# Optimization experiments

Hardware: AMD Instinct MI355X
Metric: run time of the kernel (lower is better)

The kernel has to match this reference:

```python
import jax, jax.numpy as jnp
import numpy as np

IN_F, OUT_F = 128, 128
R, LEV, N = 2, 2, 8192
JD = (R - 1) * LEV + 1  # 3 filter levels


def setup_inputs() -> dict:
    key = jax.random.key(0)
    ks = jax.random.split(key, 7)
    x = jax.random.normal(ks[0], (N, IN_F), dtype=jnp.float32)
    d_list = jax.random.uniform(ks[1], (JD, N), dtype=jnp.float32)
    U = jax.random.normal(ks[2], (N, N), dtype=jnp.float32)
    Vt = jax.random.normal(ks[3], (N, N), dtype=jnp.float32)
    # learned params
    bound = float(np.sqrt(6.0 / (IN_F + OUT_F)))  # xavier_uniform
    weight = jax.random.uniform(ks[4], (IN_F, OUT_F), dtype=jnp.float32, minval=-bound, maxval=bound)
    filt = jax.random.uniform(ks[5], (JD, N), dtype=jnp.float32, minval=0.9, maxval=1.1)
    bias = jnp.zeros((OUT_F,), dtype=jnp.float32)
    return {"x": x, "d_list": d_list, "U": U, "Vt": Vt, "weight": weight, "filt": filt, "bias": bias}


def reference(x, d_list, U, Vt, weight, filt, bias):
    # Original loop: sum_j U @ ((d_j * f_j * d_j)[:, None] * (Vt @ (x @ W)))
    # By linearity this equals U @ ((sum_j d_j^2 * f_j)[:, None] * (Vt @ (x @ W)))
    # -- same math, with Vt@xw computed once and U applied once.
    xw = x @ weight                                  # [N, out]
    Vxw = Vt @ xw                                    # [N, out]
    scale = jnp.sum(d_list * filt * d_list, axis=0)  # [N]
    out = U @ (scale[:, None] * Vxw)                 # [N, out]
    return out + bias
```

## Files before the change

### kernel.cpp

```cpp
#include <hip/hip_runtime.h>

typedef short s8v __attribute__((ext_vector_type(8)));
typedef float f32x4 __attribute__((ext_vector_type(4)));
typedef unsigned short u16x4 __attribute__((ext_vector_type(4)));

#define KC 64
#define PAD 72

__device__ __forceinline__ unsigned short f2bf(float x) {
    unsigned int u = __float_as_uint(x);
    u += 0x7fffu + ((u >> 16) & 1u);
    return (unsigned short)(u >> 16);
}

__device__ __forceinline__ s8v cvt_frag(const float4 lo, const float4 hi) {
    s8v r;
    r[0] = (short)f2bf(lo.x); r[1] = (short)f2bf(lo.y);
    r[2] = (short)f2bf(lo.z); r[3] = (short)f2bf(lo.w);
    r[4] = (short)f2bf(hi.x); r[5] = (short)f2bf(hi.y);
    r[6] = (short)f2bf(hi.z); r[7] = (short)f2bf(hi.w);
    return r;
}

__device__ __forceinline__ void gemm_core(
    const float* __restrict__ A, int lda,
    const unsigned short* __restrict__ Bt, int ldb,
    int mbase, int k0, int klen, f32x4 acc[2][4])
{
    const int t    = threadIdx.x;
    const int w    = t >> 6;
    const int lane = t & 63;
    const int quad = lane >> 4;
    const int l16  = lane & 15;
    const int mh   = w >> 1;
    const int nh   = w & 1;

    const float* rA0 = A + (size_t)(mbase + mh * 32 + l16) * lda + k0 + quad * 8;
    const float* rA1 = rA0 + (size_t)16 * lda;
    const unsigned short* rB = Bt + (size_t)(nh * 64 + l16) * ldb + k0 + quad * 8;
    const size_t bstep = (size_t)16 * ldb;

    float4 a[2][2][2][2];
    s8v    b[2][2][4];
    const int nchunks = klen / KC;

#define LOADC(s, c) do { const size_t o = (size_t)(c) * KC;                    \
        _Pragma("unroll")                                                      \
        for (int kk = 0; kk < 2; ++kk) {                                       \
            a[s][0][kk][0] = *(const float4*)(rA0 + o + kk * 32);              \
            a[s][0][kk][1] = *(const float4*)(rA0 + o + kk * 32 + 4);          \
            a[s][1][kk][0] = *(const float4*)(rA1 + o + kk * 32);              \
            a[s][1][kk][1] = *(const float4*)(rA1 + o + kk * 32 + 4);          \
        }                                                                      \
        _Pragma("unroll")                                                      \
        for (int kk = 0; kk < 2; ++kk)                                         \
            _Pragma("unroll")                                                  \
            for (int ct = 0; ct < 4; ++ct)                                     \
                b[s][kk][ct] = *(const s8v*)(rB + ct * bstep + o + kk * 32);   \
    } while (0)

#define ITER(p)                                                                \
    {                                                                          \
        _Pragma("unroll")                                                      \
        for (int kk = 0; kk < 2; ++kk) {                                       \
            s8v af0 = cvt_frag(a[p][0][kk][0], a[p][0][kk][1]);                \
            s8v af1 = cvt_frag(a[p][1][kk][0], a[p][1][kk][1]);                \
            _Pragma("unroll")                                                  \
            for (int ct = 0; ct < 4; ++ct) {                                   \
                acc[0][ct] = __builtin_amdgcn_mfma_f32_16x16x32_bf16(          \
                    af0, b[p][kk][ct], acc[0][ct], 0, 0, 0);                   \
                acc[1][ct] = __builtin_amdgcn_mfma_f32_16x16x32_bf16(          \
                    af1, b[p][kk][ct], acc[1][ct], 0, 0, 0);                   \
            }                                                                  \
        }                                                                      \
        if (c + 2 < nchunks) LOADC(p, c + 2);                                  \
    }

    LOADC(0, 0);
    if (nchunks > 1) LOADC(1, 1);
    int c = 0;
    while (true) {
        ITER(0)
        if (++c == nchunks) break;
        ITER(1)
        if (++c == nchunks) break;
    }
#undef ITER
#undef LOADC
}

__global__ __launch_bounds__(256, 2) void gemm_kernel(
    const float* __restrict__ A, int lda,
    const unsigned short* __restrict__ Bt, int ldb,
    float* __restrict__ C, int klen)
{
    f32x4 acc[2][4];
    #pragma unroll
    for (int rt = 0; rt < 2; ++rt)
        #pragma unroll
        for (int ct = 0; ct < 4; ++ct)
            acc[rt][ct] = (f32x4){0.f, 0.f, 0.f, 0.f};

    const int mbase = blockIdx.x * 64;
    gemm_core(A, lda, Bt, ldb, mbase, blockIdx.y * klen, klen, acc);

    C += (size_t)blockIdx.y * 8192 * 128;
    const int t = threadIdx.x;
    const int lane = t & 63, w = t >> 6;
    const int quad = lane >> 4, l16 = lane & 15;
    const int mh = w >> 1, nh = w & 1;
    #pragma unroll
    for (int rt = 0; rt < 2; ++rt) {
        const int row0 = mbase + mh * 32 + rt * 16 + quad * 4;
        #pragma unroll
        for (int ct = 0; ct < 4; ++ct) {
            const int col = nh * 64 + ct * 16 + l16;
            #pragma unroll
            for (int i = 0; i < 4; ++i)
                C[(size_t)(row0 + i) * 128 + col] = acc[rt][ct][i];
        }
    }
}

__global__ __launch_bounds__(256, 2) void gemm_xw_kernel(
    const float* __restrict__ x, const unsigned short* __restrict__ Wt,
    unsigned short* __restrict__ out)
{
    f32x4 acc[2][4];
    #pragma unroll
    for (int rt = 0; rt < 2; ++rt)
        #pragma unroll
        for (int ct = 0; ct < 4; ++ct)
            acc[rt][ct] = (f32x4){0.f, 0.f, 0.f, 0.f};

    const int mbase = blockIdx.x * 64;
    gemm_core(x, 128, Wt, 128, mbase, 0, 128, acc);

    const int t = threadIdx.x;
    const int lane = t & 63, w = t >> 6;
    const int quad = lane >> 4, l16 = lane & 15;
    const int mh = w >> 1, nh = w & 1;
    #pragma unroll
    for (int rt = 0; rt < 2; ++rt) {
        const int r0 = mbase + mh * 32 + rt * 16 + quad * 4;
        #pragma unroll
        for (int ct = 0; ct < 4; ++ct) {
            const int f = nh * 64 + ct * 16 + l16;
            u16x4 v;
            v[0] = f2bf(acc[rt][ct][0]); v[1] = f2bf(acc[rt][ct][1]);
            v[2] = f2bf(acc[rt][ct][2]); v[3] = f2bf(acc[rt][ct][3]);
            *(u16x4*)&out[(size_t)f * 8192 + r0] = v;
        }
    }
}

__global__ __launch_bounds__(256) void tkern(
    const float* __restrict__ a, int nslabs,
    const float* __restrict__ dl, const float* __restrict__ ft,
    unsigned short* __restrict__ out, int nrows, int mode)
{
    __shared__ __align__(16) unsigned short L[128 * PAD];
    const int t    = threadIdx.x;
    const int kb   = blockIdx.x * 64;
    const int kloc = t >> 2;
    const int fseg = (t & 3) * 32;
    const int k    = kb + kloc;
    const size_t slab = (size_t)nrows * 128;

    float s = 1.0f;
    if (mode) {
        float s0 = 0.f;
        #pragma unroll
        for (int j = 0; j < 3; ++j) {
            float d = dl[(size_t)j * nrows + k];
            s0 += d * d * ft[(size_t)j * nrows + k];
        }
        s = s0;
    }
    const float* ap = a + (size_t)k * 128 + fseg;
    #pragma unroll
    for (int i = 0; i < 8; ++i) {
        float4 v = *(const float4*)(ap + i * 4);
        for (int sl = 1; sl < nslabs; ++sl) {
            float4 u = *(const float4*)(ap + sl * slab + i * 4);
            v.x += u.x; v.y += u.y; v.z += u.z; v.w += u.w;
        }
        const int fb = fseg + i * 4;
        L[(fb + 0) * PAD + kloc] = f2bf(v.x * s);
        L[(fb + 1) * PAD + kloc] = f2bf(v.y * s);
        L[(fb + 2) * PAD + kloc] = f2bf(v.z * s);
        L[(fb + 3) * PAD + kloc] = f2bf(v.w * s);
    }
    __syncthreads();
    const int f    = t >> 1;
    const int half = (t & 1) * 32;
    unsigned short* op = out + (size_t)f * nrows + kb + half;
    #pragma unroll
    for (int i = 0; i < 4; ++i) {
        *(s8v*)(op + i * 8) = *(const s8v*)&L[f * PAD + half + i * 8];
    }
}

__global__ __launch_bounds__(256) void addbias_kernel(
    const float* __restrict__ p, const float* __restrict__ bias,
    float* __restrict__ out)
{
    const size_t e = ((size_t)blockIdx.x * 256 + threadIdx.x) * 4;
    const size_t slab = (size_t)8192 * 128;
    float4 r = *(const float4*)(bias + (e & 127));
    #pragma unroll
    for (int s = 0; s < 4; ++s) {
        float4 x = *(const float4*)(p + s * slab + e);
        r.x += x.x; r.y += x.y; r.z += x.z; r.w += x.w;
    }
    *(float4*)(out + e) = r;
}

extern "C" void kernel_launch(void* const* d_in, const int* in_sizes, int n_in,
                              void* d_out, int out_size, void* d_ws, size_t ws_size,
                              hipStream_t stream)
{
    const float* x  = (const float*)d_in[0];
    const float* dl = (const float*)d_in[1];
    const float* U  = (const float*)d_in[2];
    const float* Vt = (const float*)d_in[3];
    const float* W  = (const float*)d_in[4];
    const float* ft = (const float*)d_in[5];
    const float* bs = (const float*)d_in[6];
    float* out = (float*)d_out;

    const int N = 8192;
    const int SPLITK = 4;
    char* ws = (char*)d_ws;
    unsigned short* Wt  = (unsigned short*)(ws);
    unsigned short* xwt = (unsigned short*)(ws + (64 << 10));
    unsigned short* yt  = (unsigned short*)(ws + (64 << 10) + (2 << 20));
    float* bufA = (float*)(ws + (64 << 10) + (4 << 20));
    float* bufB = (float*)(ws + (64 << 10) + (20 << 20));

    tkern<<<dim3(2), 256, 0, stream>>>(W, 1, nullptr, nullptr, Wt, 128, 0);
    gemm_xw_kernel<<<dim3(N / 64), 256, 0, stream>>>(x, Wt, xwt);
    gemm_kernel<<<dim3(N / 64, SPLITK), 256, 0, stream>>>(Vt, N, xwt, N, bufB, N / SPLITK);
    tkern<<<dim3(N / 64), 256, 0, stream>>>(bufB, SPLITK, dl, ft, yt, N, 1);
    gemm_kernel<<<dim3(N / 64, SPLITK), 256, 0, stream>>>(U, N, yt, N, bufA, N / SPLITK);
    addbias_kernel<<<dim3((N * 128) / (256 * 4)), 256, 0, stream>>>(bufA, bs, out);
}
```

Measured before the change: 671.8 us.

## Stage GEMM tiles through LDS ring with direct global-to-LDS loads

Replaces register-prefetched global loads with a three-stage LDS ring filled by global_load_lds DMA, using XOR-swizzled layouts to avoid bank conflicts, and halves the K chunk to fit. Each wave then reads A (fp32) and B (bf16) fragments from LDS, converts A to bf16 and issues MFMAs, synchronised by explicit waitcnt plus barrier. The aim is to lower register pressure and the cost of the loads on these memory-bound skinny GEMMs. The price is a block barrier on every chunk and 48KB of LDS per block, which may limit occupancy.

Result: faster. 612.4 us (-8.8%).

```diff
diff --git a/kernel.cpp b/kernel.cpp
--- a/kernel.cpp
+++ b/kernel.cpp
@@ -4,7 +4,7 @@
 typedef float f32x4 __attribute__((ext_vector_type(4)));
 typedef unsigned short u16x4 __attribute__((ext_vector_type(4)));
 
-#define KC 64
+#define KC 32
 #define PAD 72
 
 __device__ __forceinline__ unsigned short f2bf(float x) {
@@ -13,20 +13,29 @@
     return (unsigned short)(u >> 16);
 }
 
-__device__ __forceinline__ s8v cvt_frag(const float4 lo, const float4 hi) {
+__device__ __forceinline__ s8v cvt8(const f32x4 lo, const f32x4 hi) {
     s8v r;
-    r[0] = (short)f2bf(lo.x); r[1] = (short)f2bf(lo.y);
-    r[2] = (short)f2bf(lo.z); r[3] = (short)f2bf(lo.w);
-    r[4] = (short)f2bf(hi.x); r[5] = (short)f2bf(hi.y);
-    r[6] = (short)f2bf(hi.z); r[7] = (short)f2bf(hi.w);
+    r[0] = (short)f2bf(lo[0]); r[1] = (short)f2bf(lo[1]);
+    r[2] = (short)f2bf(lo[2]); r[3] = (short)f2bf(lo[3]);
+    r[4] = (short)f2bf(hi[0]); r[5] = (short)f2bf(hi[1]);
+    r[6] = (short)f2bf(hi[2]); r[7] = (short)f2bf(hi[3]);
     return r;
 }
 
-__device__ __forceinline__ void gemm_core(
+__device__ __forceinline__ void gl2lds16(const void* g, void* l) {
+    __builtin_amdgcn_global_load_lds(
+        (const __attribute__((address_space(1))) unsigned int*)g,
+        (__attribute__((address_space(3))) unsigned int*)l, 16, 0, 0);
+}
+
+template<int EPI>
+__global__ __launch_bounds__(256, 2) void gemm_dma(
     const float* __restrict__ A, int lda,
     const unsigned short* __restrict__ Bt, int ldb,
-    int mbase, int k0, int klen, f32x4 acc[2][4])
-{
+    void* __restrict__ Cout, int klen, int Mtot)
+{
+    __shared__ __align__(16) unsigned char ring[3][16384];
+
     const int t    = threadIdx.x;
     const int w    = t >> 6;
     const int lane = t & 63;
@@ -35,65 +44,40 @@
     const int mh   = w >> 1;
     const int nh   = w & 1;
 
-    const float* rA0 = A + (size_t)(mbase + mh * 32 + l16) * lda + k0 + quad * 8;
-    const float* rA1 = rA0 + (size_t)16 * lda;
-    const unsigned short* rB = Bt + (size_t)(nh * 64 + l16) * ldb + k0 + quad * 8;
-    const size_t bstep = (size_t)16 * ldb;
-
-    float4 a[2][2][2][2];
-    s8v    b[2][2][4];
+    const int mbase   = blockIdx.x * 64;
+    const int k0      = blockIdx.y * klen;
     const int nchunks = klen / KC;
 
-#define LOADC(s, c) do { const size_t o = (size_t)(c) * KC;                    \
-        _Pragma("unroll")                                                      \
-        for (int kk = 0; kk < 2; ++kk) {                                       \
-            a[s][0][kk][0] = *(const float4*)(rA0 + o + kk * 32);              \
-            a[s][0][kk][1] = *(const float4*)(rA0 + o + kk * 32 + 4);          \
-            a[s][1][kk][0] = *(const float4*)(rA1 + o + kk * 32);              \
-            a[s][1][kk][1] = *(const float4*)(rA1 + o + kk * 32 + 4);          \
-        }                                                                      \
-        _Pragma("unroll")                                                      \
-        for (int kk = 0; kk < 2; ++kk)                                         \
-            _Pragma("unroll")                                                  \
-            for (int ct = 0; ct < 4; ++ct)                                     \
-                b[s][kk][ct] = *(const s8v*)(rB + ct * bstep + o + kk * 32);   \
+    int arow[2], aoff[2];
+    #pragma unroll
+    for (int j = 0; j < 2; ++j) {
+        const int r = (j * 4 + w) * 8 + (lane >> 3);
+        arow[j] = r;
+        aoff[j] = (((lane & 7) ^ (r & 7)) * 4);
+    }
+    int bnrow[2], bnoff[2];
+    #pragma unroll
+    for (int j = 0; j < 2; ++j) {
+        const int n = (j * 4 + w) * 16 + (lane >> 2);
+        bnrow[j] = n;
+        bnoff[j] = (((lane & 3) ^ (n & 3)) * 8);
+    }
+    const float* Abase = A + (size_t)mbase * lda + k0;
+    const int ldsoff0 = (0 * 4 + w) * 1024 + lane * 16;
+    const int ldsoff1 = (1 * 4 + w) * 1024 + lane * 16;
+
+#define ISSUE(s, c) do {                                                       \
+        const int co_ = (c) * KC;                                              \
+        gl2lds16(Abase + (size_t)arow[0] * lda + co_ + aoff[0],                \
+                 &ring[s][ldsoff0]);                                           \
+        gl2lds16(Abase + (size_t)arow[1] * lda + co_ + aoff[1],                \
+                 &ring[s][ldsoff1]);                                           \
+        gl2lds16(Bt + (size_t)bnrow[0] * ldb + k0 + co_ + bnoff[0],            \
+                 &ring[s][8192 + ldsoff0]);                                    \
+        gl2lds16(Bt + (size_t)bnrow[1] * ldb + k0 + co_ + bnoff[1],            \
+                 &ring[s][8192 + ldsoff1]);                                    \
     } while (0)
 
-#define ITER(p)                                                                \
-    {                                                                          \
-        _Pragma("unroll")                                                      \
-        for (int kk = 0; kk < 2; ++kk) {                                       \
-            s8v af0 = cvt_frag(a[p][0][kk][0], a[p][0][kk][1]);                \
-            s8v af1 = cvt_frag(a[p][1][kk][0], a[p][1][kk][1]);                \
-            _Pragma("unroll")                                                  \
-            for (int ct = 0; ct < 4; ++ct) {                                   \
-                acc[0][ct] = __builtin_amdgcn_mfma_f32_16x16x32_bf16(          \
-                    af0, b[p][kk][ct], acc[0][ct], 0, 0, 0);                   \
-                acc[1][ct] = __builtin_amdgcn_mfma_f32_16x16x32_bf16(          \
-                    af1, b[p][kk][ct], acc[1][ct], 0, 0, 0);                   \
-            }                                                                  \
-        }                                                                      \
-        if (c + 2 < nchunks) LOADC(p, c + 2);                                  \
-    }
-
-    LOADC(0, 0);
-    if (nchunks > 1) LOADC(1, 1);
-    int c = 0;
-    while (true) {
-        ITER(0)
-        if (++c == nchunks) break;
-        ITER(1)
-        if (++c == nchunks) break;
-    }
-#undef ITER
-#undef LOADC
-}
-
-__global__ __launch_bounds__(256, 2) void gemm_kernel(
-    const float* __restrict__ A, int lda,
-    const unsigned short* __restrict__ Bt, int ldb,
-    float* __restrict__ C, int klen)
-{
     f32x4 acc[2][4];
     #pragma unroll
     for (int rt = 0; rt < 2; ++rt)
@@ -101,55 +85,72 @@
         for (int ct = 0; ct < 4; ++ct)
             acc[rt][ct] = (f32x4){0.f, 0.f, 0.f, 0.f};
 
-    const int mbase = blockIdx.x * 64;
-    gemm_core(A, lda, Bt, ldb, mbase, blockIdx.y * klen, klen, acc);
-
-    C += (size_t)blockIdx.y * 8192 * 128;
-    const int t = threadIdx.x;
-    const int lane = t & 63, w = t >> 6;
-    const int quad = lane >> 4, l16 = lane & 15;
-    const int mh = w >> 1, nh = w & 1;
-    #pragma unroll
-    for (int rt = 0; rt < 2; ++rt) {
-        const int row0 = mbase + mh * 32 + rt * 16 + quad * 4;
+    ISSUE(0, 0);
+    ISSUE(1, 1);
+
+    const int aph0 = (quad * 2 + 0);
+    const int aph1 = (quad * 2 + 1);
+    const int asw  = l16 & 7;
+    const int bsw  = l16 & 3;
+
+    for (int c = 0; c < nchunks; ++c) {
+        const int s = c % 3;
+        if (c + 1 < nchunks)
+            asm volatile("s_waitcnt vmcnt(4) lgkmcnt(0)\n\ts_barrier" ::: "memory");
+        else
+            asm volatile("s_waitcnt vmcnt(0) lgkmcnt(0)\n\ts_barrier" ::: "memory");
+        if (c + 2 < nchunks) ISSUE((c + 2) % 3, c + 2);
+
+        const unsigned char* sa = &ring[s][0];
+        const unsigned char* sb = &ring[s][8192];
+        s8v af[2], bfr[4];
+        #pragma unroll
+        for (int rt = 0; rt < 2; ++rt) {
+            const int row = mh * 32 + rt * 16 + l16;
+            f32x4 lo = *(const f32x4*)(sa + row * 128 + ((aph0 ^ asw) * 16));
+            f32x4 hi = *(const f32x4*)(sa + row * 128 + ((aph1 ^ asw) * 16));
+            af[rt] = cvt8(lo, hi);
+        }
         #pragma unroll
         for (int ct = 0; ct < 4; ++ct) {
-            const int col = nh * 64 + ct * 16 + l16;
+            const int n = nh * 64 + ct * 16 + l16;
+            bfr[ct] = *(const s8v*)(sb + n * 64 + ((quad ^ bsw) * 16));
+        }
+        #pragma unroll
+        for (int rt = 0; rt < 2; ++rt)
             #pragma unroll
-            for (int i = 0; i < 4; ++i)
-                C[(size_t)(row0 + i) * 128 + col] = acc[rt][ct][i];
-        }
-    }
-}
-
-__global__ __launch_bounds__(256, 2) void gemm_xw_kernel(
-    const float* __restrict__ x, const unsigned short* __restrict__ Wt,
-    unsigned short* __restrict__ out)
-{
-    f32x4 acc[2][4];
-    #pragma unroll
-    for (int rt = 0; rt < 2; ++rt)
-        #pragma unroll
-        for (int ct = 0; ct < 4; ++ct)
-            acc[rt][ct] = (f32x4){0.f, 0.f, 0.f, 0.f};
-
-    const int mbase = blockIdx.x * 64;
-    gemm_core(x, 128, Wt, 128, mbase, 0, 128, acc);
-
-    const int t = threadIdx.x;
-    const int lane = t & 63, w = t >> 6;
-    const int quad = lane >> 4, l16 = lane & 15;
-    const int mh = w >> 1, nh = w & 1;
-    #pragma unroll
-    for (int rt = 0; rt < 2; ++rt) {
-        const int r0 = mbase + mh * 32 + rt * 16 + quad * 4;
-        #pragma unroll
-        for (int ct = 0; ct < 4; ++ct) {
-            const int f = nh * 64 + ct * 16 + l16;
-            u16x4 v;
-            v[0] = f2bf(acc[rt][ct][0]); v[1] = f2bf(acc[rt][ct][1]);
-            v[2] = f2bf(acc[rt][ct][2]); v[3] = f2bf(acc[rt][ct][3]);
-            *(u16x4*)&out[(size_t)f * 8192 + r0] = v;
+            for (int ct = 0; ct < 4; ++ct)
+                acc[rt][ct] = __builtin_amdgcn_mfma_f32_16x16x32_bf16(
+                    af[rt], bfr[ct], acc[rt][ct], 0, 0, 0);
+    }
+#undef ISSUE
+
+    if (EPI == 0) {
+        float* C = (float*)Cout + (size_t)blockIdx.y * Mtot * 128;
+        #pragma unroll
+        for (int rt = 0; rt < 2; ++rt) {
+            const int row0 = mbase + mh * 32 + rt * 16 + quad * 4;
+            #pragma unroll
+            for (int ct = 0; ct < 4; ++ct) {
+                const int col = nh * 64 + ct * 16 + l16;
+                #pragma unroll
+                for (int i = 0; i < 4; ++i)
+                    C[(size_t)(row0 + i) * 128 + col] = acc[rt][ct][i];
+            }
+        }
+    } else {
+        unsigned short* O = (unsigned short*)Cout;
+        #pragma unroll
+        for (int rt = 0; rt < 2; ++rt) {
+            const int r0 = mbase + mh * 32 + rt * 16 + quad * 4;
+            #pragma unroll
+            for (int ct = 0; ct < 4; ++ct) {
+                const int f = nh * 64 + ct * 16 + l16;
+                u16x4 v;
+                v[0] = f2bf(acc[rt][ct][0]); v[1] = f2bf(acc[rt][ct][1]);
+                v[2] = f2bf(acc[rt][ct][2]); v[3] = f2bf(acc[rt][ct][3]);
+                *(u16x4*)&O[(size_t)f * Mtot + r0] = v;
+            }
         }
     }
 }
@@ -239,9 +240,9 @@
     float* bufB = (float*)(ws + (64 << 10) + (20 << 20));
 
     tkern<<<dim3(2), 256, 0, stream>>>(W, 1, nullptr, nullptr, Wt, 128, 0);
-    gemm_xw_kernel<<<dim3(N / 64), 256, 0, stream>>>(x, Wt, xwt);
-    gemm_kernel<<<dim3(N / 64, SPLITK), 256, 0, stream>>>(Vt, N, xwt, N, bufB, N / SPLITK);
+    gemm_dma<1><<<dim3(N / 64, 1), 256, 0, stream>>>(x, 128, Wt, 128, xwt, 128, N);
+    gemm_dma<0><<<dim3(N / 64, SPLITK), 256, 0, stream>>>(Vt, N, xwt, N, bufB, N / SPLITK, N);
     tkern<<<dim3(N / 64), 256, 0, stream>>>(bufB, SPLITK, dl, ft, yt, N, 1);
-    gemm_kernel<<<dim3(N / 64, SPLITK), 256, 0, stream>>>(U, N, yt, N, bufA, N / SPLITK);
+    gemm_dma<0><<<dim3(N / 64, SPLITK), 256, 0, stream>>>(U, N, yt, N, bufA, N / SPLITK, N);
     addbias_kernel<<<dim3((N * 128) / (256 * 4)), 256, 0, stream>>>(bufA, bs, out);
 }
```
